# Optimization experiments

Hardware: AMD Instinct MI355X
Metric: run time of the kernel (lower is better)

## Reference

```python
import jax, jax.numpy as jnp
import numpy as np

IN_F, OUT_F = 128, 128
B, N = 4, 4096

def setup_inputs() -> dict:
    key = jax.random.key(0)
    k1, k2, k3 = jax.random.split(key, 3)
    relation_matrix = jax.random.uniform(k1, (B, N, N), dtype=jnp.float32)
    inputs = jax.random.normal(k2, (B, N, IN_F), dtype=jnp.float32)
    w = jax.random.normal(k3, (IN_F, OUT_F), dtype=jnp.float32)
    return {"relation_matrix": relation_matrix, "inputs": inputs, "w": w}

def reference(relation_matrix, inputs, w):
    # deg_i = sum_j A_ij ; D = diag(deg) + I  -> inverse is elementwise reciprocal
    deg = jnp.sum(relation_matrix, axis=-1) + 1.0            # [B, N]
    # (A + I) @ X  == A @ X + X  (avoids materializing A + eye)
    ax = jnp.einsum('bnm,bmf->bnf', relation_matrix, inputs) + inputs  # [B, N, in]
    z = (ax / deg[..., None]) @ w                            # [B, N, out]
    return jax.nn.relu(z)
```

## Files before the change

### kernel.cpp

```cpp
#include <hip/hip_runtime.h>
#include <hip/hip_bf16.h>
#include <stdint.h>

#define NN 4096
#define NF 128
#define NB 4

typedef __attribute__((ext_vector_type(4))) float  floatx4;
typedef __attribute__((ext_vector_type(8))) __bf16 bf16x8;

__global__ __launch_bounds__(256) void prep_kernel(const float* __restrict__ X,
                                                   const float* __restrict__ w,
                                                   __bf16* __restrict__ Xpack,
                                                   __bf16* __restrict__ wpack) {
    __shared__ float Xs[32][129];
    const int tid = threadIdx.x;
    const int bx  = blockIdx.x;
    if (bx == 512) {
        for (int p = tid; p < 512; p += 256) {
            int kc = p >> 7, n = p & 127;
#pragma unroll
            for (int k8 = 0; k8 < 32; k8 += 8) {
                bf16x8 v;
#pragma unroll
                for (int j = 0; j < 8; j++)
                    v[j] = (__bf16)w[(size_t)(kc * 32 + k8 + j) * NF + n];
                *(bf16x8*)(wpack + ((size_t)(kc * 128 + n)) * 32 + k8) = v;
            }
        }
        return;
    }
    const int b  = bx >> 7;
    const int kc = bx & 127;
    const float* Xt = X + ((size_t)b * NN + (size_t)kc * 32) * NF;
#pragma unroll
    for (int j = 0; j < 16; j++) {
        int i = tid + j * 256;
        Xs[i >> 7][i & 127] = Xt[i];
    }
    __syncthreads();
    const int f  = tid >> 1;
    const int kh = (tid & 1) * 16;
    bf16x8 v0, v1;
#pragma unroll
    for (int j = 0; j < 8; j++) v0[j] = (__bf16)Xs[kh + j][f];
#pragma unroll
    for (int j = 0; j < 8; j++) v1[j] = (__bf16)Xs[kh + 8 + j][f];
    __bf16* op = Xpack + (((size_t)b * 128 + kc) * 128 + f) * 32 + kh;
    *(bf16x8*)op = v0;
    *(bf16x8*)(op + 8) = v1;
}

__global__ __launch_bounds__(256, 3) void main_kernel(const float* __restrict__ A,
                                                      const float* __restrict__ X,
                                                      const __bf16* __restrict__ Xpack,
                                                      const __bf16* __restrict__ wpack,
                                                      float* __restrict__ out) {
    __shared__ float  Pp[2][16][132];
    __shared__ float  degp[2][16];
    __shared__ __bf16 Us[32][136];

    const int tid  = threadIdx.x;
    const int wv   = tid >> 6;
    const int lane = tid & 63;
    const int lm   = lane & 15;
    const int quad = lane >> 4;
    const int rg   = wv & 1;
    const int kq   = wv >> 1;

    const int bid = blockIdx.x;
    const int swz = (bid & 7) * 64 + (bid >> 3);
    const int b   = swz >> 7;
    const int m0  = (swz & 127) << 5;

    const int row = m0 + rg * 16 + lm;
    const float*  Ap = A + ((size_t)b * NN + row) * NN + kq * 2048 + quad * 8;
    const __bf16* Bp = Xpack + (size_t)(b * 128 + kq * 64) * 4096 + lm * 32 + quad * 8;

    floatx4 acc[8];
#pragma unroll
    for (int nt = 0; nt < 8; nt++) acc[nt] = (floatx4){0.f, 0.f, 0.f, 0.f};
    floatx4 dsa = {0.f, 0.f, 0.f, 0.f}, dsb = {0.f, 0.f, 0.f, 0.f};

    floatx4 alo = __builtin_nontemporal_load((const floatx4*)Ap);
    floatx4 ahi = __builtin_nontemporal_load((const floatx4*)(Ap + 4));

#pragma unroll 4
    for (int kc = 0; kc < 64; kc++) {
        const __bf16* Bf = Bp + (size_t)kc * 4096;
        bf16x8 bf[8];
#pragma unroll
        for (int nt = 0; nt < 8; nt++)
            bf[nt] = *(const bf16x8*)(Bf + nt * 512);
        floatx4 nlo = alo, nhi = ahi;
        if (kc + 1 < 64) {
            const float* An = Ap + (size_t)(kc + 1) * 32;
            nlo = __builtin_nontemporal_load((const floatx4*)An);
            nhi = __builtin_nontemporal_load((const floatx4*)(An + 4));
        }
        dsa += alo; dsb += ahi;
        bf16x8 af;
#pragma unroll
        for (int i = 0; i < 4; i++) { af[i] = (__bf16)alo[i]; af[4 + i] = (__bf16)ahi[i]; }
#pragma unroll
        for (int nt = 0; nt < 8; nt++)
            acc[nt] = __builtin_amdgcn_mfma_f32_16x16x32_bf16(af, bf[nt], acc[nt], 0, 0, 0);
        alo = nlo; ahi = nhi;
    }

    float ds = dsa[0] + dsa[1] + dsa[2] + dsa[3] + dsb[0] + dsb[1] + dsb[2] + dsb[3];
    ds += __shfl_xor(ds, 16, 64);
    ds += __shfl_xor(ds, 32, 64);

    if (kq == 1) {
#pragma unroll
        for (int nt = 0; nt < 8; nt++)
#pragma unroll
            for (int i = 0; i < 4; i++)
                Pp[rg][quad * 4 + i][nt * 16 + lm] = acc[nt][i];
        if (quad == 0) degp[rg][lm] = ds;
    }
    __syncthreads();

    if (kq == 0) {
        float dsf = ds + degp[rg][lm];
        float deg[4];
#pragma unroll
        for (int i = 0; i < 4; i++) deg[i] = __shfl(dsf, quad * 4 + i, 64) + 1.0f;
        const float* Xb = X + ((size_t)b * NN + m0 + rg * 16) * NF;
#pragma unroll
        for (int nt = 0; nt < 8; nt++) {
            int col = nt * 16 + lm;
#pragma unroll
            for (int i = 0; i < 4; i++) {
                int r = quad * 4 + i;
                float u = (acc[nt][i] + Pp[rg][r][col] + Xb[(size_t)r * NF + col]) / deg[i];
                Us[rg * 16 + r][col] = (__bf16)u;
            }
        }
    }

    bf16x8 wf[4][4];
#pragma unroll
    for (int kc2 = 0; kc2 < 4; kc2++)
#pragma unroll
        for (int nt = 0; nt < 4; nt++)
            wf[kc2][nt] = *(const bf16x8*)(wpack +
                (size_t)(kc2 * 128 + kq * 64 + nt * 16 + lm) * 32 + quad * 8);
    __syncthreads();

    floatx4 z[4];
#pragma unroll
    for (int nt = 0; nt < 4; nt++) z[nt] = (floatx4){0.f, 0.f, 0.f, 0.f};
#pragma unroll
    for (int kc2 = 0; kc2 < 4; kc2++) {
        bf16x8 ua = *(const bf16x8*)&Us[rg * 16 + lm][kc2 * 32 + quad * 8];
#pragma unroll
        for (int nt = 0; nt < 4; nt++)
            z[nt] = __builtin_amdgcn_mfma_f32_16x16x32_bf16(ua, wf[kc2][nt], z[nt], 0, 0, 0);
    }
    float* ob = out + ((size_t)b * NN + m0 + rg * 16) * NF;
#pragma unroll
    for (int nt = 0; nt < 4; nt++) {
        int col = kq * 64 + nt * 16 + lm;
#pragma unroll
        for (int i = 0; i < 4; i++) {
            float v = z[nt][i];
            ob[(size_t)(quad * 4 + i) * NF + col] = v > 0.f ? v : 0.f;
        }
    }
}

extern "C" void kernel_launch(void* const* d_in, const int* in_sizes, int n_in,
                              void* d_out, int out_size, void* d_ws, size_t ws_size,
                              hipStream_t stream) {
    const float* A = (const float*)d_in[0];
    const float* X = (const float*)d_in[1];
    const float* w = (const float*)d_in[2];
    float* out = (float*)d_out;

    __bf16* Xpack = (__bf16*)d_ws;
    __bf16* wpack = Xpack + (size_t)NB * NF * NN;

    prep_kernel<<<513, 256, 0, stream>>>(X, w, Xpack, wpack);
    main_kernel<<<512, 256, 0, stream>>>(A, X, Xpack, wpack, out);
}
```

Measured before the change: 415.4 us.

## Split K four ways per wave, each wave covering both row groups for B reuse

Each of the four waves now covers a quarter of K and both 16-row halves of the 32-row tile. Each loaded Xpack B fragment therefore feeds two MFMAs, which halves B-operand traffic per FLOP. The loop is software-pipelined with the B fragments one step ahead and the A loads two steps ahead, and the three partial accumulators are reduced through shared memory. Register pressure rises, so launch bounds drop to 2 blocks per SM, which lowers occupancy in exchange for more bytes in flight per wave and more reuse.

```diff
diff --git a/kernel.cpp b/kernel.cpp
--- a/kernel.cpp
+++ b/kernel.cpp
@@ -51,122 +51,152 @@
     *(bf16x8*)(op + 8) = v1;
 }
 
-__global__ __launch_bounds__(256, 3) void main_kernel(const float* __restrict__ A,
+__global__ __launch_bounds__(256, 2) void main_kernel(const float* __restrict__ A,
                                                       const float* __restrict__ X,
                                                       const __bf16* __restrict__ Xpack,
                                                       const __bf16* __restrict__ wpack,
                                                       float* __restrict__ out) {
-    __shared__ float  Pp[2][16][132];
-    __shared__ float  degp[2][16];
+    __shared__ float  Pacc[3][32][132];
+    __shared__ float  degp[4][32];
     __shared__ __bf16 Us[32][136];
 
     const int tid  = threadIdx.x;
-    const int wv   = tid >> 6;
+    const int kq   = tid >> 6;
     const int lane = tid & 63;
     const int lm   = lane & 15;
     const int quad = lane >> 4;
-    const int rg   = wv & 1;
-    const int kq   = wv >> 1;
 
     const int bid = blockIdx.x;
     const int swz = (bid & 7) * 64 + (bid >> 3);
     const int b   = swz >> 7;
     const int m0  = (swz & 127) << 5;
 
-    const int row = m0 + rg * 16 + lm;
-    const float*  Ap = A + ((size_t)b * NN + row) * NN + kq * 2048 + quad * 8;
-    const __bf16* Bp = Xpack + (size_t)(b * 128 + kq * 64) * 4096 + lm * 32 + quad * 8;
-
-    floatx4 acc[8];
-#pragma unroll
-    for (int nt = 0; nt < 8; nt++) acc[nt] = (floatx4){0.f, 0.f, 0.f, 0.f};
-    floatx4 dsa = {0.f, 0.f, 0.f, 0.f}, dsb = {0.f, 0.f, 0.f, 0.f};
-
-    floatx4 alo = __builtin_nontemporal_load((const floatx4*)Ap);
-    floatx4 ahi = __builtin_nontemporal_load((const floatx4*)(Ap + 4));
-
-#pragma unroll 4
-    for (int kc = 0; kc < 64; kc++) {
-        const __bf16* Bf = Bp + (size_t)kc * 4096;
-        bf16x8 bf[8];
-#pragma unroll
-        for (int nt = 0; nt < 8; nt++)
-            bf[nt] = *(const bf16x8*)(Bf + nt * 512);
-        floatx4 nlo = alo, nhi = ahi;
-        if (kc + 1 < 64) {
-            const float* An = Ap + (size_t)(kc + 1) * 32;
-            nlo = __builtin_nontemporal_load((const floatx4*)An);
-            nhi = __builtin_nontemporal_load((const floatx4*)(An + 4));
-        }
-        dsa += alo; dsb += ahi;
-        bf16x8 af;
-#pragma unroll
-        for (int i = 0; i < 4; i++) { af[i] = (__bf16)alo[i]; af[4 + i] = (__bf16)ahi[i]; }
-#pragma unroll
-        for (int nt = 0; nt < 8; nt++)
-            acc[nt] = __builtin_amdgcn_mfma_f32_16x16x32_bf16(af, bf[nt], acc[nt], 0, 0, 0);
-        alo = nlo; ahi = nhi;
-    }
-
-    float ds = dsa[0] + dsa[1] + dsa[2] + dsa[3] + dsb[0] + dsb[1] + dsb[2] + dsb[3];
-    ds += __shfl_xor(ds, 16, 64);
-    ds += __shfl_xor(ds, 32, 64);
-
-    if (kq == 1) {
-#pragma unroll
-        for (int nt = 0; nt < 8; nt++)
-#pragma unroll
-            for (int i = 0; i < 4; i++)
-                Pp[rg][quad * 4 + i][nt * 16 + lm] = acc[nt][i];
-        if (quad == 0) degp[rg][lm] = ds;
-    }
+    const float* Ap0 = A + ((size_t)b * NN + m0 + lm) * NN + kq * 1024 + quad * 8;
+    const float* Ap1 = Ap0 + (size_t)16 * NN;
+    const __bf16* Bp = Xpack + ((size_t)(b * 128 + kq * 32)) * 4096 + lm * 32 + quad * 8;
+
+    floatx4 acc[2][8];
+#pragma unroll
+    for (int s = 0; s < 2; s++)
+#pragma unroll
+        for (int nt = 0; nt < 8; nt++) acc[s][nt] = (floatx4){0.f, 0.f, 0.f, 0.f};
+    floatx4 sum0 = {0.f, 0.f, 0.f, 0.f}, sum1 = {0.f, 0.f, 0.f, 0.f};
+
+    floatx4 a00 = __builtin_nontemporal_load((const floatx4*)Ap0);
+    floatx4 a01 = __builtin_nontemporal_load((const floatx4*)(Ap0 + 4));
+    floatx4 a10 = __builtin_nontemporal_load((const floatx4*)Ap1);
+    floatx4 a11 = __builtin_nontemporal_load((const floatx4*)(Ap1 + 4));
+    floatx4 n00 = __builtin_nontemporal_load((const floatx4*)(Ap0 + 32));
+    floatx4 n01 = __builtin_nontemporal_load((const floatx4*)(Ap0 + 36));
+    floatx4 n10 = __builtin_nontemporal_load((const floatx4*)(Ap1 + 32));
+    floatx4 n11 = __builtin_nontemporal_load((const floatx4*)(Ap1 + 36));
+    bf16x8 bc[8];
+#pragma unroll
+    for (int nt = 0; nt < 8; nt++) bc[nt] = *(const bf16x8*)(Bp + nt * 512);
+
+    for (int kc = 0; kc < 32; kc++) {
+        const int kb = kc + 1 < 32 ? kc + 1 : 0;
+        const int ka = kc + 2 < 32 ? kc + 2 : 0;
+        bf16x8 bn[8];
+        const __bf16* Bf = Bp + (size_t)kb * 4096;
+#pragma unroll
+        for (int nt = 0; nt < 8; nt++) bn[nt] = *(const bf16x8*)(Bf + nt * 512);
+        const float* An0 = Ap0 + (size_t)ka * 32;
+        const float* An1 = Ap1 + (size_t)ka * 32;
+        floatx4 m00 = __builtin_nontemporal_load((const floatx4*)An0);
+        floatx4 m01 = __builtin_nontemporal_load((const floatx4*)(An0 + 4));
+        floatx4 m10 = __builtin_nontemporal_load((const floatx4*)An1);
+        floatx4 m11 = __builtin_nontemporal_load((const floatx4*)(An1 + 4));
+
+        sum0 += a00 + a01;
+        sum1 += a10 + a11;
+        bf16x8 af0, af1;
+#pragma unroll
+        for (int i = 0; i < 4; i++) { af0[i] = (__bf16)a00[i]; af0[4 + i] = (__bf16)a01[i]; }
+#pragma unroll
+        for (int i = 0; i < 4; i++) { af1[i] = (__bf16)a10[i]; af1[4 + i] = (__bf16)a11[i]; }
+#pragma unroll
+        for (int nt = 0; nt < 8; nt++) {
+            acc[0][nt] = __builtin_amdgcn_mfma_f32_16x16x32_bf16(af0, bc[nt], acc[0][nt], 0, 0, 0);
+            acc[1][nt] = __builtin_amdgcn_mfma_f32_16x16x32_bf16(af1, bc[nt], acc[1][nt], 0, 0, 0);
+        }
+        a00 = n00; a01 = n01; a10 = n10; a11 = n11;
+        n00 = m00; n01 = m01; n10 = m10; n11 = m11;
+#pragma unroll
+        for (int nt = 0; nt < 8; nt++) bc[nt] = bn[nt];
+    }
+
+    float ds0 = sum0[0] + sum0[1] + sum0[2] + sum0[3];
+    float ds1 = sum1[0] + sum1[1] + sum1[2] + sum1[3];
+    ds0 += __shfl_xor(ds0, 16, 64); ds0 += __shfl_xor(ds0, 32, 64);
+    ds1 += __shfl_xor(ds1, 16, 64); ds1 += __shfl_xor(ds1, 32, 64);
+    if (quad == 0) { degp[kq][lm] = ds0; degp[kq][16 + lm] = ds1; }
+
+    if (kq) {
+#pragma unroll
+        for (int s = 0; s < 2; s++)
+#pragma unroll
+            for (int nt = 0; nt < 8; nt++)
+#pragma unroll
+                for (int i = 0; i < 4; i++)
+                    Pacc[kq - 1][s * 16 + quad * 4 + i][nt * 16 + lm] = acc[s][nt][i];
+    }
+
+    bf16x8 wf[4][2];
+#pragma unroll
+    for (int kc2 = 0; kc2 < 4; kc2++)
+#pragma unroll
+        for (int nt = 0; nt < 2; nt++)
+            wf[kc2][nt] = *(const bf16x8*)(wpack +
+                (size_t)(kc2 * 128 + kq * 32 + nt * 16 + lm) * 32 + quad * 8);
+
     __syncthreads();
 
     if (kq == 0) {
-        float dsf = ds + degp[rg][lm];
-        float deg[4];
-#pragma unroll
-        for (int i = 0; i < 4; i++) deg[i] = __shfl(dsf, quad * 4 + i, 64) + 1.0f;
-        const float* Xb = X + ((size_t)b * NN + m0 + rg * 16) * NF;
-#pragma unroll
-        for (int nt = 0; nt < 8; nt++) {
-            int col = nt * 16 + lm;
+        float degv[2][4];
+#pragma unroll
+        for (int s = 0; s < 2; s++)
 #pragma unroll
             for (int i = 0; i < 4; i++) {
-                int r = quad * 4 + i;
-                float u = (acc[nt][i] + Pp[rg][r][col] + Xb[(size_t)r * NF + col]) / deg[i];
-                Us[rg * 16 + r][col] = (__bf16)u;
+                int r = s * 16 + quad * 4 + i;
+                degv[s][i] = degp[0][r] + degp[1][r] + degp[2][r] + degp[3][r] + 1.0f;
             }
-        }
-    }
-
-    bf16x8 wf[4][4];
-#pragma unroll
-    for (int kc2 = 0; kc2 < 4; kc2++)
-#pragma unroll
-        for (int nt = 0; nt < 4; nt++)
-            wf[kc2][nt] = *(const bf16x8*)(wpack +
-                (size_t)(kc2 * 128 + kq * 64 + nt * 16 + lm) * 32 + quad * 8);
+        const float* Xb = X + ((size_t)b * NN + m0) * NF;
+#pragma unroll
+        for (int s = 0; s < 2; s++)
+#pragma unroll
+            for (int nt = 0; nt < 8; nt++)
+#pragma unroll
+                for (int i = 0; i < 4; i++) {
+                    int r = s * 16 + quad * 4 + i, col = nt * 16 + lm;
+                    float u = acc[s][nt][i] + Pacc[0][r][col] + Pacc[1][r][col] +
+                              Pacc[2][r][col] + Xb[(size_t)r * NF + col];
+                    Us[r][col] = (__bf16)(u / degv[s][i]);
+                }
+    }
     __syncthreads();
 
-    floatx4 z[4];
-#pragma unroll
-    for (int nt = 0; nt < 4; nt++) z[nt] = (floatx4){0.f, 0.f, 0.f, 0.f};
-#pragma unroll
-    for (int kc2 = 0; kc2 < 4; kc2++) {
-        bf16x8 ua = *(const bf16x8*)&Us[rg * 16 + lm][kc2 * 32 + quad * 8];
-#pragma unroll
-        for (int nt = 0; nt < 4; nt++)
-            z[nt] = __builtin_amdgcn_mfma_f32_16x16x32_bf16(ua, wf[kc2][nt], z[nt], 0, 0, 0);
-    }
-    float* ob = out + ((size_t)b * NN + m0 + rg * 16) * NF;
-#pragma unroll
-    for (int nt = 0; nt < 4; nt++) {
-        int col = kq * 64 + nt * 16 + lm;
-#pragma unroll
-        for (int i = 0; i < 4; i++) {
-            float v = z[nt][i];
-            ob[(size_t)(quad * 4 + i) * NF + col] = v > 0.f ? v : 0.f;
+    float* ob = out + ((size_t)b * NN + m0) * NF;
+#pragma unroll
+    for (int s = 0; s < 2; s++) {
+        floatx4 z0 = {0.f, 0.f, 0.f, 0.f};
+        floatx4 z1 = {0.f, 0.f, 0.f, 0.f};
+#pragma unroll
+        for (int kc2 = 0; kc2 < 4; kc2++) {
+            bf16x8 ua = *(const bf16x8*)&Us[s * 16 + lm][kc2 * 32 + quad * 8];
+            z0 = __builtin_amdgcn_mfma_f32_16x16x32_bf16(ua, wf[kc2][0], z0, 0, 0, 0);
+            z1 = __builtin_amdgcn_mfma_f32_16x16x32_bf16(ua, wf[kc2][1], z1, 0, 0, 0);
+        }
+#pragma unroll
+        for (int nt = 0; nt < 2; nt++) {
+            int col = kq * 32 + nt * 16 + lm;
+            floatx4 zv = nt ? z1 : z0;
+#pragma unroll
+            for (int i = 0; i < 4; i++) {
+                int r = s * 16 + quad * 4 + i;
+                float v = zv[i];
+                ob[(size_t)r * NF + col] = v > 0.f ? v : 0.f;
+            }
         }
     }
 }
```

After: 391.5 us. 1.06x faster.
